# Performance work log

Hardware: AMD Instinct MI355X
Metric: run time of the kernel (lower is better)

## Reference

```python
import jax, jax.numpy as jnp
import numpy as np

H = 2048            # hidden_size
INTER = 8192        # intermediate_size
E = 16              # num_experts
V = 32000           # vocab_size
I = INTER // E      # per-expert intermediate (tp_size=1) = 512
N = 4096            # num_tokens
BASE_ROUTING_SCALE = 10.0


def setup_inputs() -> dict:
    key = jax.random.key(0)
    ks = jax.random.split(key, 6)
    x = jax.random.normal(ks[0], (N, H), dtype=jnp.float32)
    token_ids = jax.random.randint(ks[1], (N,), 0, V)
    mu = jax.random.normal(ks[2], (N, H), dtype=jnp.float32)
    # kaiming-uniform-ish scaled params
    gate_up_proj = jax.random.normal(ks[3], (E, H, 2 * I), dtype=jnp.float32) * (1.0 / np.sqrt(H))
    down_proj = jax.random.normal(ks[4], (E, I, H), dtype=jnp.float32) * (1.0 / np.sqrt(I))
    # mu_router initialized to zeros in the module; use small random so routing is actually mu-biased
    mu_router_w = jax.random.normal(ks[5], (E, H), dtype=jnp.float32) * 0.02
    return {"x": x, "token_ids": token_ids, "mu": mu,
            "gate_up_proj": gate_up_proj, "down_proj": down_proj,
            "mu_router_w": mu_router_w}


def reference(x, token_ids, mu, gate_up_proj, down_proj, mu_router_w):
    # --- routing: expert = token_id % E, biased by mu logits ---
    base = jnp.clip(token_ids, 0, V - 1) % E              # [N]
    logits = (jax.nn.one_hot(base, E, dtype=jnp.float32) * BASE_ROUTING_SCALE
              + mu @ mu_router_w.T)                       # [N, E]
    expert_ids = jnp.argmax(logits, axis=-1)              # [N]

    Iloc = gate_up_proj.shape[-1] // 2

    # --- grouped expert SwiGLU MLP: scan over experts, mask-combine outputs ---
    def step(acc, inp):
        wg, wd, e = inp
        gu = x @ wg                                       # [N, 2I]
        h = jax.nn.silu(gu[:, :Iloc]) * gu[:, Iloc:]      # [N, I]
        o = h @ wd                                        # [N, H]
        acc = acc + jnp.where((expert_ids == e)[:, None], o, 0.0)
        return acc, None

    out0 = jnp.zeros_like(x)
    out, _ = jax.lax.scan(step, out0, (gate_up_proj, down_proj, jnp.arange(E)))
    return out
```

## Files before the change

### kernel.cpp

```cpp
#include <hip/hip_runtime.h>
#include <hip/hip_bf16.h>

#define NT 4096
#define HD 2048
#define NE 16
#define ID 512
#define TWO_I 1024
#define PITCH 72
#define MAXITEMS 47

typedef __attribute__((ext_vector_type(8))) short bf16x8_t;
typedef __attribute__((ext_vector_type(4))) float f32x4_t;

__device__ __forceinline__ unsigned short f2bf(float f) {
  union { float f; unsigned int u; } v; v.f = f;
  unsigned int r = v.u + 0x7fffu + ((v.u >> 16) & 1u);
  return (unsigned short)(r >> 16);
}
__device__ __forceinline__ unsigned pk2(unsigned short a, unsigned short b) {
  return (unsigned)a | ((unsigned)b << 16);
}
__device__ __forceinline__ void gl_lds16(const void* g, void* l) {
  __builtin_amdgcn_global_load_lds(
      (const __attribute__((address_space(1))) unsigned int*)g,
      (__attribute__((address_space(3))) unsigned int*)l, 16, 0, 0);
}

__global__ void k_cast_x(const float* __restrict__ x, unsigned short* __restrict__ xb) {
  size_t i = ((size_t)blockIdx.x * 256 + threadIdx.x) * 8;
  float4 a = *(const float4*)(x + i);
  float4 b = *(const float4*)(x + i + 4);
  uint4 pk;
  pk.x = pk2(f2bf(a.x), f2bf(a.y)); pk.y = pk2(f2bf(a.z), f2bf(a.w));
  pk.z = pk2(f2bf(b.x), f2bf(b.y)); pk.w = pk2(f2bf(b.z), f2bf(b.w));
  *(uint4*)(xb + i) = pk;
}

__global__ void k_route(const float* __restrict__ mu, const int* __restrict__ tok,
                        const float* __restrict__ wr, int* __restrict__ eid) {
  int t = blockIdx.x;
  int tid = threadIdx.x;
  float p[NE];
#pragma unroll
  for (int e = 0; e < NE; ++e) p[e] = 0.f;
  const float* m = mu + (size_t)t * HD;
  for (int h = tid; h < HD; h += 256) {
    float mv = m[h];
#pragma unroll
    for (int e = 0; e < NE; ++e) p[e] += mv * wr[e * HD + h];
  }
#pragma unroll
  for (int e = 0; e < NE; ++e) {
    float v = p[e];
#pragma unroll
    for (int s = 32; s; s >>= 1) v += __shfl_xor(v, s, 64);
    p[e] = v;
  }
  __shared__ float red[4][NE];
  int lane = tid & 63, wv = tid >> 6;
  if (lane == 0) {
#pragma unroll
    for (int e = 0; e < NE; ++e) red[wv][e] = p[e];
  }
  __syncthreads();
  if (tid == 0) {
    int tk = tok[t];
    if (tk < 0) tk = 0;
    if (tk > 31999) tk = 31999;
    int base = tk & 15;
    float best = -3.0e38f; int bi = 0;
    for (int e = 0; e < NE; ++e) {
      float v = red[0][e] + red[1][e] + red[2][e] + red[3][e];
      if (e == base) v += 10.0f;
      if (v > best) { best = v; bi = e; }
    }
    eid[t] = bi;
  }
}

__global__ void k_init(int* counts, int* cursors) {
  int i = threadIdx.x;
  if (i < NE) { counts[i] = 0; cursors[i] = 0; }
}
__global__ void k_hist(const int* __restrict__ eid, int* __restrict__ counts) {
  int t = blockIdx.x * 256 + threadIdx.x;
  if (t < NT) atomicAdd(&counts[eid[t]], 1);
}
__global__ void k_scan(const int* __restrict__ counts, int* __restrict__ offsets,
                       int* __restrict__ cursors, int* __restrict__ wk) {
  if (threadIdx.x == 0) {
    int s = 0;
    for (int e = 0; e < NE; ++e) { offsets[e] = s; cursors[e] = s; s += counts[e]; }
    offsets[NE] = s;
    int n = 0;
    for (int e = 0; e < NE; ++e) {
      int tiles = (counts[e] + 127) >> 7;
      for (int m = 0; m < tiles; ++m) { wk[n++] = e | (m << 8); }
    }
    wk[MAXITEMS] = n;
  }
}
__global__ void k_scatter(const int* __restrict__ eid, int* __restrict__ cursors,
                          int* __restrict__ tlist) {
  int t = blockIdx.x * 256 + threadIdx.x;
  if (t < NT) {
    int e = eid[t];
    int pos = atomicAdd(&cursors[e], 1);
    tlist[pos] = t;
  }
}

__global__ __launch_bounds__(256, 2) void k_gemm1(
    const unsigned short* __restrict__ xb, const float* __restrict__ gup,
    const int* __restrict__ offsets, const int* __restrict__ tlist,
    const int* __restrict__ wk, unsigned short* __restrict__ hbuf) {
  int item = blockIdx.y;
  if (item >= wk[MAXITEMS]) return;
  int w = wk[item];
  int e = w & 255, tb = (w >> 8) * 128;
  int off = offsets[e], cnt = offsets[e + 1] - off;
  int c0 = blockIdx.x * 32;

  __shared__ unsigned short Abuf[2][128 * 64];
  __shared__ float Bbuf[2][64 * 64];
  __shared__ unsigned short Pbuf[64 * PITCH];
  __shared__ int ltok[128];

  int tid = threadIdx.x, lane = tid & 63, wv = tid >> 6;
  if (tid < 128) { int r = tb + tid; if (r > cnt - 1) r = cnt - 1; ltok[tid] = tlist[off + r]; }
  __syncthreads();

  const unsigned short* aSrc[4];
  int aDst[4];
  int cswz = (lane & 7) ^ ((lane >> 3) & 7);
#pragma unroll
  for (int i = 0; i < 4; ++i) {
    int r = wv * 32 + i * 8 + (lane >> 3);
    aSrc[i] = xb + (size_t)ltok[r] * HD + cswz * 8;
    aDst[i] = (wv * 32 + i * 8) * 64;
  }
  const float* bSrc[4];
  int bDst[4];
  {
    int cc = lane & 15;
    int gcol = (cc < 8) ? (c0 + cc * 4) : (ID + c0 + (cc - 8) * 4);
    const float* Wg = gup + (size_t)e * HD * TWO_I;
#pragma unroll
    for (int i = 0; i < 4; ++i) {
      int kr = wv * 16 + i * 4 + (lane >> 4);
      bSrc[i] = Wg + (size_t)kr * TWO_I + gcol;
      bDst[i] = (wv * 16 + i * 4) * 64;
    }
  }

  auto stage = [&](int buf) {
#pragma unroll
    for (int i = 0; i < 4; ++i) { gl_lds16(aSrc[i], &Abuf[buf][aDst[i]]); aSrc[i] += 64; }
#pragma unroll
    for (int i = 0; i < 4; ++i) { gl_lds16(bSrc[i], &Bbuf[buf][bDst[i]]); bSrc[i] += (size_t)64 * TWO_I; }
  };

  stage(0);

  f32x4_t zero = {0.f, 0.f, 0.f, 0.f};
  f32x4_t accg[2][2], accu[2][2];
#pragma unroll
  for (int m = 0; m < 2; ++m)
#pragma unroll
    for (int n = 0; n < 2; ++n) { accg[m][n] = zero; accu[m][n] = zero; }

  int lr = lane & 15, hi = lane >> 4, mb = wv * 32;

  for (int kt = 0; kt < 32; ++kt) {
    int cur = kt & 1;
    if (kt < 31) {
      stage(cur ^ 1);
      asm volatile("s_waitcnt vmcnt(8)" ::: "memory");
    } else {
      asm volatile("s_waitcnt vmcnt(0)" ::: "memory");
    }
    __builtin_amdgcn_sched_barrier(0);
    __builtin_amdgcn_s_barrier();

    {
      int c = lane, ks = wv;
      unsigned short tmp[16];
#pragma unroll
      for (int j = 0; j < 16; ++j) tmp[j] = f2bf(Bbuf[cur][(ks * 16 + j) * 64 + c]);
      uint4 p0, p1;
      p0.x = pk2(tmp[0], tmp[1]);   p0.y = pk2(tmp[2], tmp[3]);
      p0.z = pk2(tmp[4], tmp[5]);   p0.w = pk2(tmp[6], tmp[7]);
      p1.x = pk2(tmp[8], tmp[9]);   p1.y = pk2(tmp[10], tmp[11]);
      p1.z = pk2(tmp[12], tmp[13]); p1.w = pk2(tmp[14], tmp[15]);
      *(uint4*)&Pbuf[c * PITCH + ks * 16] = p0;
      *(uint4*)&Pbuf[c * PITCH + ks * 16 + 8] = p1;
    }
    asm volatile("s_waitcnt lgkmcnt(0)" ::: "memory");
    __builtin_amdgcn_sched_barrier(0);
    __builtin_amdgcn_s_barrier();

#pragma unroll
    for (int kk = 0; kk < 2; ++kk) {
      int klo = kk * 32 + hi * 8;
      bf16x8_t a[2], bg[2], bu[2];
#pragma unroll
      for (int m = 0; m < 2; ++m) {
        int R = mb + m * 16 + lr;
        int ch = (kk * 4 + hi) ^ (R & 7);
        a[m] = *(bf16x8_t*)&Abuf[cur][R * 64 + ch * 8];
      }
#pragma unroll
      for (int n = 0; n < 2; ++n) {
        bg[n] = *(bf16x8_t*)&Pbuf[(n * 16 + lr) * PITCH + klo];
        bu[n] = *(bf16x8_t*)&Pbuf[(32 + n * 16 + lr) * PITCH + klo];
      }
#pragma unroll
      for (int m = 0; m < 2; ++m)
#pragma unroll
        for (int n = 0; n < 2; ++n) {
          accg[m][n] = __builtin_amdgcn_mfma_f32_16x16x32_bf16(a[m], bg[n], accg[m][n], 0, 0, 0);
          accu[m][n] = __builtin_amdgcn_mfma_f32_16x16x32_bf16(a[m], bu[n], accu[m][n], 0, 0, 0);
        }
    }
    if (kt < 31) __builtin_amdgcn_s_barrier();
  }

  int rq = hi * 4;
#pragma unroll
  for (int m = 0; m < 2; ++m)
#pragma unroll
    for (int n = 0; n < 2; ++n)
#pragma unroll
      for (int j = 0; j < 4; ++j) {
        int r = tb + mb + m * 16 + rq + j;
        if (r < cnt) {
          float g = accg[m][n][j], u = accu[m][n][j];
          float hv = (g / (1.f + __expf(-g))) * u;
          hbuf[(size_t)(off + r) * ID + c0 + n * 16 + lr] = f2bf(hv);
        }
      }
}

__global__ __launch_bounds__(256, 2) void k_gemm2(
    const unsigned short* __restrict__ hbuf, const float* __restrict__ dwn,
    const int* __restrict__ offsets, const int* __restrict__ tlist,
    const int* __restrict__ wk, float* __restrict__ out) {
  int item = blockIdx.y;
  if (item >= wk[MAXITEMS]) return;
  int w = wk[item];
  int e = w & 255, tb = (w >> 8) * 128;
  int off = offsets[e], cnt = offsets[e + 1] - off;
  int c0 = blockIdx.x * 64;

  __shared__ unsigned short Abuf[2][128 * 64];
  __shared__ float Bbuf[2][64 * 64];
  __shared__ unsigned short Pbuf[64 * PITCH];

  int tid = threadIdx.x, lane = tid & 63, wv = tid >> 6;

  const unsigned short* aSrc[4];
  int aDst[4];
  int cswz = (lane & 7) ^ ((lane >> 3) & 7);
#pragma unroll
  for (int i = 0; i < 4; ++i) {
    int r = tb + wv * 32 + i * 8 + (lane >> 3);
    if (r > cnt - 1) r = cnt - 1;
    aSrc[i] = hbuf + (size_t)(off + r) * ID + cswz * 8;
    aDst[i] = (wv * 32 + i * 8) * 64;
  }
  const float* bSrc[4];
  int bDst[4];
  {
    int cc = lane & 15;
    const float* Wd = dwn + (size_t)e * ID * HD;
#pragma unroll
    for (int i = 0; i < 4; ++i) {
      int kr = wv * 16 + i * 4 + (lane >> 4);
      bSrc[i] = Wd + (size_t)kr * HD + c0 + cc * 4;
      bDst[i] = (wv * 16 + i * 4) * 64;
    }
  }

  auto stage = [&](int buf) {
#pragma unroll
    for (int i = 0; i < 4; ++i) { gl_lds16(aSrc[i], &Abuf[buf][aDst[i]]); aSrc[i] += 64; }
#pragma unroll
    for (int i = 0; i < 4; ++i) { gl_lds16(bSrc[i], &Bbuf[buf][bDst[i]]); bSrc[i] += (size_t)64 * HD; }
  };

  stage(0);

  f32x4_t zero = {0.f, 0.f, 0.f, 0.f};
  f32x4_t acc[2][4];
#pragma unroll
  for (int m = 0; m < 2; ++m)
#pragma unroll
    for (int n = 0; n < 4; ++n) acc[m][n] = zero;

  int lr = lane & 15, hi = lane >> 4, mb = wv * 32;

  for (int kt = 0; kt < 8; ++kt) {
    int cur = kt & 1;
    if (kt < 7) {
      stage(cur ^ 1);
      asm volatile("s_waitcnt vmcnt(8)" ::: "memory");
    } else {
      asm volatile("s_waitcnt vmcnt(0)" ::: "memory");
    }
    __builtin_amdgcn_sched_barrier(0);
    __builtin_amdgcn_s_barrier();

    {
      int c = lane, ks = wv;
      unsigned short tmp[16];
#pragma unroll
      for (int j = 0; j < 16; ++j) tmp[j] = f2bf(Bbuf[cur][(ks * 16 + j) * 64 + c]);
      uint4 p0, p1;
      p0.x = pk2(tmp[0], tmp[1]);   p0.y = pk2(tmp[2], tmp[3]);
      p0.z = pk2(tmp[4], tmp[5]);   p0.w = pk2(tmp[6], tmp[7]);
      p1.x = pk2(tmp[8], tmp[9]);   p1.y = pk2(tmp[10], tmp[11]);
      p1.z = pk2(tmp[12], tmp[13]); p1.w = pk2(tmp[14], tmp[15]);
      *(uint4*)&Pbuf[c * PITCH + ks * 16] = p0;
      *(uint4*)&Pbuf[c * PITCH + ks * 16 + 8] = p1;
    }
    asm volatile("s_waitcnt lgkmcnt(0)" ::: "memory");
    __builtin_amdgcn_sched_barrier(0);
    __builtin_amdgcn_s_barrier();

#pragma unroll
    for (int kk = 0; kk < 2; ++kk) {
      int klo = kk * 32 + hi * 8;
      bf16x8_t a[2], b[4];
#pragma unroll
      for (int m = 0; m < 2; ++m) {
        int R = mb + m * 16 + lr;
        int ch = (kk * 4 + hi) ^ (R & 7);
        a[m] = *(bf16x8_t*)&Abuf[cur][R * 64 + ch * 8];
      }
#pragma unroll
      for (int n = 0; n < 4; ++n) b[n] = *(bf16x8_t*)&Pbuf[(n * 16 + lr) * PITCH + klo];
#pragma unroll
      for (int m = 0; m < 2; ++m)
#pragma unroll
        for (int n = 0; n < 4; ++n)
          acc[m][n] = __builtin_amdgcn_mfma_f32_16x16x32_bf16(a[m], b[n], acc[m][n], 0, 0, 0);
    }
    if (kt < 7) __builtin_amdgcn_s_barrier();
  }

  int rq = hi * 4;
#pragma unroll
  for (int m = 0; m < 2; ++m)
#pragma unroll
    for (int n = 0; n < 4; ++n)
#pragma unroll
      for (int j = 0; j < 4; ++j) {
        int r = tb + mb + m * 16 + rq + j;
        if (r < cnt) {
          out[(size_t)tlist[off + r] * HD + c0 + n * 16 + lr] = acc[m][n][j];
        }
      }
}

extern "C" void kernel_launch(void* const* d_in, const int* in_sizes, int n_in,
                              void* d_out, int out_size, void* d_ws, size_t ws_size,
                              hipStream_t stream) {
  (void)in_sizes; (void)n_in; (void)out_size; (void)ws_size;
  const float* x   = (const float*)d_in[0];
  const int*   tok = (const int*)d_in[1];
  const float* mu  = (const float*)d_in[2];
  const float* gup = (const float*)d_in[3];
  const float* dwn = (const float*)d_in[4];
  const float* wr  = (const float*)d_in[5];
  float* out = (float*)d_out;

  char* ws = (char*)d_ws;
  int* eid     = (int*)ws;
  int* tlist   = (int*)(ws + 16384);
  int* counts  = (int*)(ws + 32768);
  int* offsets = (int*)(ws + 32896);
  int* cursors = (int*)(ws + 33024);
  int* wk      = (int*)(ws + 33152);
  unsigned short* xb   = (unsigned short*)(ws + 65536);
  unsigned short* hbuf = (unsigned short*)(ws + 65536 + (size_t)NT * HD * 2);

  k_cast_x <<<4096, 256, 0, stream>>>(x, xb);
  k_route  <<<NT, 256, 0, stream>>>(mu, tok, wr, eid);
  k_init   <<<1, 64, 0, stream>>>(counts, cursors);
  k_hist   <<<16, 256, 0, stream>>>(eid, counts);
  k_scan   <<<1, 64, 0, stream>>>(counts, offsets, cursors, wk);
  k_scatter<<<16, 256, 0, stream>>>(eid, cursors, tlist);
  k_gemm1  <<<dim3(16, MAXITEMS), 256, 0, stream>>>(xb, gup, offsets, tlist, wk, hbuf);
  k_gemm2  <<<dim3(32, MAXITEMS), 256, 0, stream>>>(hbuf, dwn, offsets, tlist, wk, out);
}
```

Before: 220.9 us.

## Load A operand directly into registers and drop LDS A staging

Both grouped GEMM kernels now read the activation (A) fragments straight from global memory into registers each k-step instead of staging them through a swizzled LDS double buffer. Only the fp32 weight tile still goes through LDS. Freeing the A buffers shrinks LDS use, which lets launch bounds rise from 2 to 3 blocks per SM, and the MFMA section runs at raised wave priority. The loop barriers and waitcnts were reordered to match. The risk is that the direct loads, which are not coalesced across waves and are issued with no prefetch ahead, add global latency that the extra occupancy has to hide.

```diff
diff --git a/kernel.cpp b/kernel.cpp
--- a/kernel.cpp
+++ b/kernel.cpp
@@ -110,7 +110,7 @@
   }
 }
 
-__global__ __launch_bounds__(256, 2) void k_gemm1(
+__global__ __launch_bounds__(256, 3) void k_gemm1(
     const unsigned short* __restrict__ xb, const float* __restrict__ gup,
     const int* __restrict__ offsets, const int* __restrict__ tlist,
     const int* __restrict__ wk, unsigned short* __restrict__ hbuf) {
@@ -121,7 +121,6 @@
   int off = offsets[e], cnt = offsets[e + 1] - off;
   int c0 = blockIdx.x * 32;
 
-  __shared__ unsigned short Abuf[2][128 * 64];
   __shared__ float Bbuf[2][64 * 64];
   __shared__ unsigned short Pbuf[64 * PITCH];
   __shared__ int ltok[128];
@@ -130,15 +129,10 @@
   if (tid < 128) { int r = tb + tid; if (r > cnt - 1) r = cnt - 1; ltok[tid] = tlist[off + r]; }
   __syncthreads();
 
-  const unsigned short* aSrc[4];
-  int aDst[4];
-  int cswz = (lane & 7) ^ ((lane >> 3) & 7);
-#pragma unroll
-  for (int i = 0; i < 4; ++i) {
-    int r = wv * 32 + i * 8 + (lane >> 3);
-    aSrc[i] = xb + (size_t)ltok[r] * HD + cswz * 8;
-    aDst[i] = (wv * 32 + i * 8) * 64;
-  }
+  int lr = lane & 15, hi = lane >> 4, mb = wv * 32;
+  const unsigned short* aRow0 = xb + (size_t)ltok[mb + lr] * HD + hi * 8;
+  const unsigned short* aRow1 = xb + (size_t)ltok[mb + 16 + lr] * HD + hi * 8;
+
   const float* bSrc[4];
   int bDst[4];
   {
@@ -152,15 +146,12 @@
       bDst[i] = (wv * 16 + i * 4) * 64;
     }
   }
-
-  auto stage = [&](int buf) {
-#pragma unroll
-    for (int i = 0; i < 4; ++i) { gl_lds16(aSrc[i], &Abuf[buf][aDst[i]]); aSrc[i] += 64; }
+  auto stageB = [&](int buf) {
 #pragma unroll
     for (int i = 0; i < 4; ++i) { gl_lds16(bSrc[i], &Bbuf[buf][bDst[i]]); bSrc[i] += (size_t)64 * TWO_I; }
   };
 
-  stage(0);
+  stageB(0);
 
   f32x4_t zero = {0.f, 0.f, 0.f, 0.f};
   f32x4_t accg[2][2], accu[2][2];
@@ -169,16 +160,19 @@
 #pragma unroll
     for (int n = 0; n < 2; ++n) { accg[m][n] = zero; accu[m][n] = zero; }
 
-  int lr = lane & 15, hi = lane >> 4, mb = wv * 32;
-
   for (int kt = 0; kt < 32; ++kt) {
     int cur = kt & 1;
-    if (kt < 31) {
-      stage(cur ^ 1);
-      asm volatile("s_waitcnt vmcnt(8)" ::: "memory");
-    } else {
-      asm volatile("s_waitcnt vmcnt(0)" ::: "memory");
-    }
+    __builtin_amdgcn_s_barrier();
+    bf16x8_t a00, a01, a10, a11;
+    a00 = *(const bf16x8_t*)(aRow0 + kt * 64);
+    a01 = *(const bf16x8_t*)(aRow0 + kt * 64 + 32);
+    a10 = *(const bf16x8_t*)(aRow1 + kt * 64);
+    a11 = *(const bf16x8_t*)(aRow1 + kt * 64 + 32);
+    __builtin_amdgcn_sched_barrier(0);
+    if (kt < 31) stageB(cur ^ 1);
+    __builtin_amdgcn_sched_barrier(0);
+    if (kt < 31) asm volatile("s_waitcnt vmcnt(4)" ::: "memory");
+    else         asm volatile("s_waitcnt vmcnt(0)" ::: "memory");
     __builtin_amdgcn_sched_barrier(0);
     __builtin_amdgcn_s_barrier();
 
@@ -199,30 +193,27 @@
     __builtin_amdgcn_sched_barrier(0);
     __builtin_amdgcn_s_barrier();
 
+    __builtin_amdgcn_s_setprio(1);
 #pragma unroll
     for (int kk = 0; kk < 2; ++kk) {
       int klo = kk * 32 + hi * 8;
-      bf16x8_t a[2], bg[2], bu[2];
-#pragma unroll
-      for (int m = 0; m < 2; ++m) {
-        int R = mb + m * 16 + lr;
-        int ch = (kk * 4 + hi) ^ (R & 7);
-        a[m] = *(bf16x8_t*)&Abuf[cur][R * 64 + ch * 8];
-      }
+      bf16x8_t bg[2], bu[2];
 #pragma unroll
       for (int n = 0; n < 2; ++n) {
         bg[n] = *(bf16x8_t*)&Pbuf[(n * 16 + lr) * PITCH + klo];
         bu[n] = *(bf16x8_t*)&Pbuf[(32 + n * 16 + lr) * PITCH + klo];
       }
-#pragma unroll
-      for (int m = 0; m < 2; ++m)
-#pragma unroll
-        for (int n = 0; n < 2; ++n) {
-          accg[m][n] = __builtin_amdgcn_mfma_f32_16x16x32_bf16(a[m], bg[n], accg[m][n], 0, 0, 0);
-          accu[m][n] = __builtin_amdgcn_mfma_f32_16x16x32_bf16(a[m], bu[n], accu[m][n], 0, 0, 0);
-        }
-    }
-    if (kt < 31) __builtin_amdgcn_s_barrier();
+      bf16x8_t a0 = kk ? a01 : a00;
+      bf16x8_t a1 = kk ? a11 : a10;
+#pragma unroll
+      for (int n = 0; n < 2; ++n) {
+        accg[0][n] = __builtin_amdgcn_mfma_f32_16x16x32_bf16(a0, bg[n], accg[0][n], 0, 0, 0);
+        accu[0][n] = __builtin_amdgcn_mfma_f32_16x16x32_bf16(a0, bu[n], accu[0][n], 0, 0, 0);
+        accg[1][n] = __builtin_amdgcn_mfma_f32_16x16x32_bf16(a1, bg[n], accg[1][n], 0, 0, 0);
+        accu[1][n] = __builtin_amdgcn_mfma_f32_16x16x32_bf16(a1, bu[n], accu[1][n], 0, 0, 0);
+      }
+    }
+    __builtin_amdgcn_s_setprio(0);
   }
 
   int rq = hi * 4;
@@ -241,7 +232,7 @@
       }
 }
 
-__global__ __launch_bounds__(256, 2) void k_gemm2(
+__global__ __launch_bounds__(256, 3) void k_gemm2(
     const unsigned short* __restrict__ hbuf, const float* __restrict__ dwn,
     const int* __restrict__ offsets, const int* __restrict__ tlist,
     const int* __restrict__ wk, float* __restrict__ out) {
@@ -252,22 +243,17 @@
   int off = offsets[e], cnt = offsets[e + 1] - off;
   int c0 = blockIdx.x * 64;
 
-  __shared__ unsigned short Abuf[2][128 * 64];
   __shared__ float Bbuf[2][64 * 64];
   __shared__ unsigned short Pbuf[64 * PITCH];
 
   int tid = threadIdx.x, lane = tid & 63, wv = tid >> 6;
-
-  const unsigned short* aSrc[4];
-  int aDst[4];
-  int cswz = (lane & 7) ^ ((lane >> 3) & 7);
-#pragma unroll
-  for (int i = 0; i < 4; ++i) {
-    int r = tb + wv * 32 + i * 8 + (lane >> 3);
-    if (r > cnt - 1) r = cnt - 1;
-    aSrc[i] = hbuf + (size_t)(off + r) * ID + cswz * 8;
-    aDst[i] = (wv * 32 + i * 8) * 64;
-  }
+  int lr = lane & 15, hi = lane >> 4, mb = wv * 32;
+
+  int r0 = tb + mb + lr;      if (r0 > cnt - 1) r0 = cnt - 1;
+  int r1 = tb + mb + 16 + lr; if (r1 > cnt - 1) r1 = cnt - 1;
+  const unsigned short* aRow0 = hbuf + (size_t)(off + r0) * ID + hi * 8;
+  const unsigned short* aRow1 = hbuf + (size_t)(off + r1) * ID + hi * 8;
+
   const float* bSrc[4];
   int bDst[4];
   {
@@ -280,15 +266,12 @@
       bDst[i] = (wv * 16 + i * 4) * 64;
     }
   }
-
-  auto stage = [&](int buf) {
-#pragma unroll
-    for (int i = 0; i < 4; ++i) { gl_lds16(aSrc[i], &Abuf[buf][aDst[i]]); aSrc[i] += 64; }
+  auto stageB = [&](int buf) {
 #pragma unroll
     for (int i = 0; i < 4; ++i) { gl_lds16(bSrc[i], &Bbuf[buf][bDst[i]]); bSrc[i] += (size_t)64 * HD; }
   };
 
-  stage(0);
+  stageB(0);
 
   f32x4_t zero = {0.f, 0.f, 0.f, 0.f};
   f32x4_t acc[2][4];
@@ -297,16 +280,19 @@
 #pragma unroll
     for (int n = 0; n < 4; ++n) acc[m][n] = zero;
 
-  int lr = lane & 15, hi = lane >> 4, mb = wv * 32;
-
   for (int kt = 0; kt < 8; ++kt) {
     int cur = kt & 1;
-    if (kt < 7) {
-      stage(cur ^ 1);
-      asm volatile("s_waitcnt vmcnt(8)" ::: "memory");
-    } else {
-      asm volatile("s_waitcnt vmcnt(0)" ::: "memory");
-    }
+    __builtin_amdgcn_s_barrier();
+    bf16x8_t a00, a01, a10, a11;
+    a00 = *(const bf16x8_t*)(aRow0 + kt * 64);
+    a01 = *(const bf16x8_t*)(aRow0 + kt * 64 + 32);
+    a10 = *(const bf16x8_t*)(aRow1 + kt * 64);
+    a11 = *(const bf16x8_t*)(aRow1 + kt * 64 + 32);
+    __builtin_amdgcn_sched_barrier(0);
+    if (kt < 7) stageB(cur ^ 1);
+    __builtin_amdgcn_sched_barrier(0);
+    if (kt < 7) asm volatile("s_waitcnt vmcnt(4)" ::: "memory");
+    else        asm volatile("s_waitcnt vmcnt(0)" ::: "memory");
     __builtin_amdgcn_sched_barrier(0);
     __builtin_amdgcn_s_barrier();
 
@@ -327,25 +313,22 @@
     __builtin_amdgcn_sched_barrier(0);
     __builtin_amdgcn_s_barrier();
 
+    __builtin_amdgcn_s_setprio(1);
 #pragma unroll
     for (int kk = 0; kk < 2; ++kk) {
       int klo = kk * 32 + hi * 8;
-      bf16x8_t a[2], b[4];
-#pragma unroll
-      for (int m = 0; m < 2; ++m) {
-        int R = mb + m * 16 + lr;
-        int ch = (kk * 4 + hi) ^ (R & 7);
-        a[m] = *(bf16x8_t*)&Abuf[cur][R * 64 + ch * 8];
-      }
+      bf16x8_t b[4];
 #pragma unroll
       for (int n = 0; n < 4; ++n) b[n] = *(bf16x8_t*)&Pbuf[(n * 16 + lr) * PITCH + klo];
-#pragma unroll
-      for (int m = 0; m < 2; ++m)
-#pragma unroll
-        for (int n = 0; n < 4; ++n)
-          acc[m][n] = __builtin_amdgcn_mfma_f32_16x16x32_bf16(a[m], b[n], acc[m][n], 0, 0, 0);
-    }
-    if (kt < 7) __builtin_amdgcn_s_barrier();
+      bf16x8_t a0 = kk ? a01 : a00;
+      bf16x8_t a1 = kk ? a11 : a10;
+#pragma unroll
+      for (int n = 0; n < 4; ++n) {
+        acc[0][n] = __builtin_amdgcn_mfma_f32_16x16x32_bf16(a0, b[n], acc[0][n], 0, 0, 0);
+        acc[1][n] = __builtin_amdgcn_mfma_f32_16x16x32_bf16(a1, b[n], acc[1][n], 0, 0, 0);
+      }
+    }
+    __builtin_amdgcn_s_setprio(0);
   }
 
   int rq = hi * 4;
```

After: 202.8 us. 8.2% less time.
